# Performance work log

Measured on AMD Instinct MI355X. Metric: run time of the kernel, lower is better.

The kernel has to match this reference:

```python
import jax, jax.numpy as jnp
import numpy as np


def setup_inputs() -> dict:
    key = jax.random.key(0)
    ks = jax.random.split(key, 6)
    B, S, DK = 4, 2048, 1024
    scale = 1.0 / np.sqrt(DK)  # keep weight magnitudes sane like torch init
    return {
        "q": jax.random.normal(ks[0], (B, S, DK), jnp.float32),
        "k": jax.random.normal(ks[1], (B, S, DK), jnp.float32),
        "v": jax.random.normal(ks[2], (B, S, DK), jnp.float32),
        "wq": jax.random.normal(ks[3], (DK, DK), jnp.float32) * scale,
        "wk": jax.random.normal(ks[4], (DK, DK), jnp.float32) * scale,
        "wv": jax.random.normal(ks[5], (DK, DK), jnp.float32) * scale,
    }


def reference(q, k, v, wq, wk, wv):
    dk = q.shape[-1]
    # nn.Linear: y = x @ W^T  (weights stored [out, in])
    qp = jnp.einsum("bsd,ed->bse", q, wq)
    kp = jnp.einsum("bsd,ed->bse", k, wk)
    vp = jnp.einsum("bsd,ed->bse", v, wv)
    norm = 1.0 / jnp.sqrt(jnp.asarray(dk, qp.dtype))
    s = jnp.einsum("bqd,bkd->bqk", qp, kp) * norm  # [B, S, S]
    # module computes exp(s)/sum(exp(s)) manually; mathematically softmax
    e = jnp.exp(s)
    attention = e / jnp.sum(e, axis=-1, keepdims=True)
    # dropout is identity in eval mode (deterministic reference)
    return jnp.einsum("bqk,bkd->bqd", attention, vp)
```

## Files before the change

kernel.cpp:

```cpp
#include <hip/hip_runtime.h>

typedef _Float16 f16;
typedef _Float16 f16x4 __attribute__((ext_vector_type(4)));
typedef _Float16 f16x8 __attribute__((ext_vector_type(8)));
typedef float    fx4   __attribute__((ext_vector_type(4)));

#define MODE_PROJ   0
#define MODE_SCORES 1
#define MODE_PV     2

constexpr int Bsz = 4;
constexpr int S   = 2048;
constexpr int DK  = 1024;
constexpr int BM = 128, BN = 128, BK = 64;
constexpr long SD   = (long)S * DK;
constexpr long SS   = (long)S * S;
constexpr long BIGN = (long)Bsz * S * DK;

__device__ __forceinline__ void glds16(const f16* g, f16* l) {
    __builtin_amdgcn_global_load_lds(
        (const __attribute__((address_space(1))) void*)g,
        (__attribute__((address_space(3))) void*)l, 16, 0, 0);
}

template<int SH>
__device__ __forceinline__ size_t pp(int r, int c) {
    return ((size_t)(r >> 1) << SH) + ((r & 1) << 10) + c;
}

__global__ __launch_bounds__(256)
void convert_kernel(const float* q, const float* k, const float* v,
                    const float* wq, const float* wk, const float* wv,
                    f16* dq, f16* dk, f16* dv,
                    f16* dwq, f16* dwk, f16* dwv,
                    int sh, int inplace, float* rowsum)
{
    const int tid = threadIdx.x;
    if (blockIdx.x < 8) {
        float4 zz = {0.f, 0.f, 0.f, 0.f};
        *(float4*)&rowsum[(blockIdx.x * 256 + tid) * 4] = zz;
    }
    float4 f0[4], f1[4];
    f16* dst[4];
    size_t doff[4];
    #pragma unroll
    for (int i = 0; i < 4; ++i) {
        int cx = blockIdx.x + i * 3456;
        const float* s; f16* d; int blk;
        if (cx < 12288) {
            int t = cx >> 12; blk = cx & 4095;
            s = (t == 0) ? q : (t == 1) ? k : v;
            d = (t == 0) ? dq : (t == 1) ? dk : dv;
        } else {
            int u = cx - 12288;
            int t = u >> 9; blk = u & 511;
            s = (t == 0) ? wq : (t == 1) ? wk : wv;
            d = (t == 0) ? dwq : (t == 1) ? dwk : dwv;
        }
        size_t off = (size_t)blk * 2048 + (size_t)tid * 8;
        f0[i] = *(const float4*)(s + off);
        f1[i] = *(const float4*)(s + off + 4);
        dst[i]  = d;
        doff[i] = ((size_t)blk << (sh + 1)) + (size_t)tid * 16;
    }
    if (inplace) __syncthreads();
    #pragma unroll
    for (int i = 0; i < 4; ++i) {
        f16x8 h = {(f16)f0[i].x, (f16)f0[i].y, (f16)f0[i].z, (f16)f0[i].w,
                   (f16)f1[i].x, (f16)f1[i].y, (f16)f1[i].z, (f16)f1[i].w};
        *(f16x8*)((char*)dst[i] + doff[i]) = h;
    }
}

template<int MODE, int SH>
__global__ __launch_bounds__(256, 4)
void gemm_kernel(const f16* A0, const f16* A1, const f16* A2,
                 const f16* B0, const f16* B1, const f16* B2,
                 void* O0, void* O1, float* rowsum,
                 int lda, int ldb, int K, int ldo, int zz)
{
    __shared__ f16 lA[BM * BK];
    __shared__ f16 lB[BN * BK];

    const int tid = threadIdx.x;
    int id, z;
    if constexpr (MODE == MODE_PROJ) {
        id = blockIdx.x;
        z  = (zz >= 0) ? zz : (int)blockIdx.y;
    } else {
        constexpr int PB = (MODE == MODE_SCORES) ? 256 : 128;
        int f = blockIdx.x;
        int g = (f & 7) * ((PB * Bsz) >> 3) + (f >> 3);
        z  = g / PB;
        id = g % PB;
    }
    int row0, col0;
    if constexpr (MODE == MODE_PROJ) { row0 = (id & 63) * BM; col0 = (id >> 6) * BN; }
    else                             { row0 = (id & 15) * BM; col0 = (id >> 4) * BN; }

    const int lane = tid & 63;
    const int quad = lane >> 4;
    const int cn   = lane & 15;
    const int w    = tid >> 6;
    const int wm   = w >> 1;
    const int wn   = w & 1;

    const f16 *Ap, *Bp;
    if constexpr (MODE == MODE_PROJ) {
        Ap = (z == 0) ? A0 : (z == 1) ? A1 : A2;
        Bp = (z == 0) ? B0 : (z == 1) ? B1 : B2;
    } else if constexpr (MODE == MODE_SCORES) {
        Ap = A0 + (long)z * SD;  Bp = B0 + (long)z * SD;
        rowsum += (long)z * S;
    } else {
        Ap = A0 + (long)z * SS;  Bp = B0 + (long)z * SD;
        rowsum += (long)z * S;
    }

    fx4 acc[4][4];
    #pragma unroll
    for (int mt = 0; mt < 4; ++mt)
        #pragma unroll
        for (int nt = 0; nt < 4; ++nt)
            acc[mt][nt] = (fx4){0.f, 0.f, 0.f, 0.f};

    const int lr8 = lane >> 3;
    const int swc = (lane & 7) ^ lr8;
    const int lcS = swc << 3;

    for (int k0 = 0; k0 < K; k0 += BK) {
        __syncthreads();
        #pragma unroll
        for (int i = 0; i < 4; ++i) {
            int rb = w * 32 + i * 8;
            if constexpr (MODE == MODE_PROJ) {
                glds16(Ap + pp<SH>(row0 + rb + lr8, k0 + lcS), &lA[rb * BK]);
                glds16(Bp + pp<SH>(col0 + rb + lr8, k0 + lcS), &lB[rb * BK]);
            } else {
                glds16(Ap + (size_t)(row0 + rb + lr8) * lda + k0 + lcS, &lA[rb * BK]);
                glds16(Bp + (size_t)(col0 + rb + lr8) * ldb + k0 + lcS, &lB[rb * BK]);
            }
        }
        __syncthreads();

        #pragma unroll
        for (int kh = 0; kh < 2; ++kh) {
            f16x8 af[4], bf[4];
            #pragma unroll
            for (int mt = 0; mt < 4; ++mt) {
                int r = wm * 64 + mt * 16 + cn;
                int ch = ((kh << 2) | quad) ^ (r & 7);
                af[mt] = *(const f16x8*)&lA[r * BK + ch * 8];
            }
            #pragma unroll
            for (int nt = 0; nt < 4; ++nt) {
                int r = wn * 64 + nt * 16 + cn;
                int ch = ((kh << 2) | quad) ^ (r & 7);
                bf[nt] = *(const f16x8*)&lB[r * BK + ch * 8];
            }
            #pragma unroll
            for (int mt = 0; mt < 4; ++mt)
                #pragma unroll
                for (int nt = 0; nt < 4; ++nt)
                    acc[mt][nt] = __builtin_amdgcn_mfma_f32_16x16x32_f16(
                        af[mt], bf[nt], acc[mt][nt], 0, 0, 0);
        }
    }

    if constexpr (MODE == MODE_PROJ) {
        if (z < 2) {
            f16* O = (f16*)O0 + (long)z * BIGN;
            #pragma unroll
            for (int mt = 0; mt < 4; ++mt) {
                int r0 = row0 + wm * 64 + mt * 16 + quad * 4;
                #pragma unroll
                for (int nt = 0; nt < 4; ++nt) {
                    int c = col0 + wn * 64 + nt * 16 + cn;
                    #pragma unroll
                    for (int reg = 0; reg < 4; ++reg)
                        O[(size_t)(r0 + reg) * DK + c] = (f16)acc[mt][nt][reg];
                }
            }
        } else {
            #pragma unroll
            for (int mt = 0; mt < 4; ++mt) {
                int r0 = row0 + wm * 64 + mt * 16 + quad * 4;
                int b  = r0 >> 11;
                int s  = r0 & 2047;
                f16* O = (f16*)O1 + (long)b * SD;
                #pragma unroll
                for (int nt = 0; nt < 4; ++nt) {
                    int c = col0 + wn * 64 + nt * 16 + cn;
                    f16x4 h = {(f16)acc[mt][nt][0], (f16)acc[mt][nt][1],
                               (f16)acc[mt][nt][2], (f16)acc[mt][nt][3]};
                    *(f16x4*)&O[(size_t)c * S + s] = h;
                }
            }
        }
    } else if constexpr (MODE == MODE_SCORES) {
        f16* O = (f16*)O0 + (long)z * SS;
        const float sl2e = 0.03125f * 1.44269504f;
        float rs[4][4];
        #pragma unroll
        for (int mt = 0; mt < 4; ++mt)
            #pragma unroll
            for (int reg = 0; reg < 4; ++reg) rs[mt][reg] = 0.f;
        #pragma unroll
        for (int mt = 0; mt < 4; ++mt) {
            int r0 = row0 + wm * 64 + mt * 16 + quad * 4;
            #pragma unroll
            for (int nt = 0; nt < 4; ++nt) {
                int c = col0 + wn * 64 + nt * 16 + cn;
                #pragma unroll
                for (int reg = 0; reg < 4; ++reg) {
                    float vv = exp2f(acc[mt][nt][reg] * sl2e);
                    rs[mt][reg] += vv;
                    O[(size_t)(r0 + reg) * ldo + c] = (f16)vv;
                }
            }
        }
        #pragma unroll
        for (int mt = 0; mt < 4; ++mt) {
            int r0 = row0 + wm * 64 + mt * 16 + quad * 4;
            #pragma unroll
            for (int reg = 0; reg < 4; ++reg) {
                float vv = rs[mt][reg];
                vv += __shfl_xor(vv, 1);
                vv += __shfl_xor(vv, 2);
                vv += __shfl_xor(vv, 4);
                vv += __shfl_xor(vv, 8);
                if (cn == 0) atomicAdd(&rowsum[r0 + reg], vv);
            }
        }
    } else {
        float* O = (float*)O0 + (long)z * SD;
        #pragma unroll
        for (int mt = 0; mt < 4; ++mt) {
            int r0 = row0 + wm * 64 + mt * 16 + quad * 4;
            fx4 rsv = *(const fx4*)&rowsum[r0];
            fx4 inv = {1.f / rsv[0], 1.f / rsv[1], 1.f / rsv[2], 1.f / rsv[3]};
            #pragma unroll
            for (int nt = 0; nt < 4; ++nt) {
                int c = col0 + wn * 64 + nt * 16 + cn;
                #pragma unroll
                for (int reg = 0; reg < 4; ++reg)
                    O[(size_t)(r0 + reg) * ldo + c] = acc[mt][nt][reg] * inv[reg];
            }
        }
    }
}

extern "C" void kernel_launch(void* const* d_in, const int* in_sizes, int n_in,
                              void* d_out, int out_size, void* d_ws, size_t ws_size,
                              hipStream_t stream) {
    const float* q  = (const float*)d_in[0];
    const float* k  = (const float*)d_in[1];
    const float* v  = (const float*)d_in[2];
    const float* wq = (const float*)d_in[3];
    const float* wk = (const float*)d_in[4];
    const float* wv = (const float*)d_in[5];
    float* out = (float*)d_out;

    char* ws = (char*)d_ws;
    f16*   qp     = (f16*)(ws);
    f16*   kp     = (f16*)(ws + ((size_t)16 << 20));
    f16*   vpT    = (f16*)(ws + ((size_t)32 << 20));
    f16*   E      = (f16*)(ws + ((size_t)48 << 20));
    float* rowsum = (float*)(ws + ((size_t)80 << 20));

    const bool usews = ws_size >= ((size_t)135 << 20);
    char* cb = ws + ((size_t)81 << 20);
    f16 *dq, *dk, *dv, *dwq, *dwk, *dwv;
    if (usews) {
        dq  = (f16*)(cb);
        dk  = (f16*)(cb + ((size_t)16 << 20));
        dv  = (f16*)(cb + ((size_t)32 << 20));
        dwq = (f16*)(cb + ((size_t)48 << 20));
        dwk = (f16*)(cb + ((size_t)50 << 20));
        dwv = (f16*)(cb + ((size_t)52 << 20));
    } else {
        dq  = (f16*)q;  dk  = (f16*)k;  dv  = (f16*)v;
        dwq = (f16*)wq; dwk = (f16*)wk; dwv = (f16*)wv;
    }

    convert_kernel<<<3456, 256, 0, stream>>>(
        q, k, v, wq, wk, wv, dq, dk, dv, dwq, dwk, dwv,
        usews ? 11 : 12, usews ? 0 : 1, rowsum);

    dim3 blk(256);
    if (usews) {
        gemm_kernel<MODE_PROJ, 11><<<512, blk, 0, stream>>>(
            dq, dk, dv, dwq, dwk, dwv, qp, vpT, nullptr, DK, DK, DK, DK, 0);
        gemm_kernel<MODE_PROJ, 11><<<512, blk, 0, stream>>>(
            dq, dk, dv, dwq, dwk, dwv, qp, vpT, nullptr, DK, DK, DK, DK, 1);
        gemm_kernel<MODE_PROJ, 11><<<512, blk, 0, stream>>>(
            dq, dk, dv, dwq, dwk, dwv, qp, vpT, nullptr, DK, DK, DK, DK, 2);
    } else {
        gemm_kernel<MODE_PROJ, 12><<<512, blk, 0, stream>>>(
            dq, dk, dv, dwq, dwk, dwv, qp, vpT, nullptr, DK, DK, DK, DK, 0);
        gemm_kernel<MODE_PROJ, 12><<<512, blk, 0, stream>>>(
            dq, dk, dv, dwq, dwk, dwv, qp, vpT, nullptr, DK, DK, DK, DK, 1);
        gemm_kernel<MODE_PROJ, 12><<<512, blk, 0, stream>>>(
            dq, dk, dv, dwq, dwk, dwv, qp, vpT, nullptr, DK, DK, DK, DK, 2);
    }
    gemm_kernel<MODE_SCORES, 12><<<1024, blk, 0, stream>>>(
        qp, nullptr, nullptr, kp, nullptr, nullptr, E, nullptr, rowsum,
        DK, DK, DK, S, -1);
    gemm_kernel<MODE_PV, 12><<<512, blk, 0, stream>>>(
        E, nullptr, nullptr, vpT, nullptr, nullptr, out, nullptr, rowsum,
        S, S, S, DK, -1);
}
```

Baseline: 305.6 us.

## Fuse fp32-to-fp16 conversion of activations into projection GEMM A-tile loads

Removes the separate conversion pass over q/k/v by having the projection GEMM load fp32 activations directly into registers, convert them, and store them into LDS, with a one-tile register prefetch. Only the weights are now pre-converted by a smaller kernel, which also zeroes rowsum. This cuts the large write and reread of fp16 activation copies, in exchange for register-staged A loads and doubled fp32 read bytes per A tile, which is re-read across column blocks.

```diff
diff --git a/kernel.cpp b/kernel.cpp
--- a/kernel.cpp
+++ b/kernel.cpp
@@ -26,6 +26,36 @@
 template<int SH>
 __device__ __forceinline__ size_t pp(int r, int c) {
     return ((size_t)(r >> 1) << SH) + ((r & 1) << 10) + c;
+}
+
+__global__ __launch_bounds__(256)
+void convert_w_kernel(const float* wq, const float* wk, const float* wv,
+                      f16* dwq, f16* dwk, f16* dwv, float* rowsum)
+{
+    const int tid = threadIdx.x;
+    const int bid = blockIdx.x;
+    if (bid < 8) {
+        float4 zz = {0.f, 0.f, 0.f, 0.f};
+        *(float4*)&rowsum[(bid * 256 + tid) * 4] = zz;
+    }
+    float4 fv[4];
+    f16*   dp[4];
+    #pragma unroll
+    for (int i = 0; i < 4; ++i) {
+        unsigned g = (unsigned)(i * 196608 + bid * 256 + tid);
+        unsigned t = g >> 18;
+        unsigned off = g & 262143u;
+        const float* s = (t == 0) ? wq : (t == 1) ? wk : wv;
+        f16* d = (t == 0) ? dwq : (t == 1) ? dwk : dwv;
+        fv[i] = *(const float4*)(s + (size_t)off * 4);
+        dp[i] = d + (size_t)off * 4;
+    }
+    __builtin_amdgcn_sched_barrier(0);
+    #pragma unroll
+    for (int i = 0; i < 4; ++i) {
+        f16x4 h = {(f16)fv[i].x, (f16)fv[i].y, (f16)fv[i].z, (f16)fv[i].w};
+        *(f16x4*)dp[i] = h;
+    }
 }
 
 __global__ __launch_bounds__(256)
@@ -72,15 +102,16 @@
     }
 }
 
-template<int MODE, int SH>
+template<int MODE, int SH, int AF32>
 __global__ __launch_bounds__(256, 4)
 void gemm_kernel(const f16* A0, const f16* A1, const f16* A2,
                  const f16* B0, const f16* B1, const f16* B2,
+                 const float* F0, const float* F1, const float* F2,
                  void* O0, void* O1, float* rowsum,
                  int lda, int ldb, int K, int ldo, int zz)
 {
-    __shared__ f16 lA[BM * BK];
-    __shared__ f16 lB[BN * BK];
+    __shared__ __attribute__((aligned(16))) f16 lA[BM * BK];
+    __shared__ __attribute__((aligned(16))) f16 lB[BN * BK];
 
     const int tid = threadIdx.x;
     int id, z;
@@ -105,9 +136,11 @@
     const int wm   = w >> 1;
     const int wn   = w & 1;
 
-    const f16 *Ap, *Bp;
+    const f16 *Ap = nullptr, *Bp = nullptr;
+    const float *Fp = nullptr;
     if constexpr (MODE == MODE_PROJ) {
-        Ap = (z == 0) ? A0 : (z == 1) ? A1 : A2;
+        if constexpr (AF32) Fp = (z == 0) ? F0 : (z == 1) ? F1 : F2;
+        else                Ap = (z == 0) ? A0 : (z == 1) ? A1 : A2;
         Bp = (z == 0) ? B0 : (z == 1) ? B1 : B2;
     } else if constexpr (MODE == MODE_SCORES) {
         Ap = A0 + (long)z * SD;  Bp = B0 + (long)z * SD;
@@ -128,20 +161,52 @@
     const int swc = (lane & 7) ^ lr8;
     const int lcS = swc << 3;
 
+    float4 pfa[8];
+#define LOADA(K0) do {                                                       \
+    _Pragma("unroll")                                                        \
+    for (int i_ = 0; i_ < 4; ++i_) {                                         \
+        const float* sp_ = Fp + (size_t)(row0 + w * 32 + i_ * 8 + lr8) * DK  \
+                              + (K0) + lcS;                                  \
+        pfa[2 * i_]     = *(const float4*)sp_;                               \
+        pfa[2 * i_ + 1] = *(const float4*)(sp_ + 4);                         \
+    }                                                                        \
+} while (0)
+
+    if constexpr (MODE == MODE_PROJ && AF32) LOADA(0);
+
     for (int k0 = 0; k0 < K; k0 += BK) {
         __syncthreads();
-        #pragma unroll
-        for (int i = 0; i < 4; ++i) {
-            int rb = w * 32 + i * 8;
-            if constexpr (MODE == MODE_PROJ) {
-                glds16(Ap + pp<SH>(row0 + rb + lr8, k0 + lcS), &lA[rb * BK]);
+        if constexpr (MODE == MODE_PROJ && AF32) {
+            #pragma unroll
+            for (int i = 0; i < 4; ++i) {
+                int rb = w * 32 + i * 8;
+                float4 a = pfa[2 * i], b = pfa[2 * i + 1];
+                f16x8 h = {(f16)a.x, (f16)a.y, (f16)a.z, (f16)a.w,
+                           (f16)b.x, (f16)b.y, (f16)b.z, (f16)b.w};
+                *(f16x8*)&lA[(rb + lr8) * BK + (lane & 7) * 8] = h;
                 glds16(Bp + pp<SH>(col0 + rb + lr8, k0 + lcS), &lB[rb * BK]);
-            } else {
-                glds16(Ap + (size_t)(row0 + rb + lr8) * lda + k0 + lcS, &lA[rb * BK]);
-                glds16(Bp + (size_t)(col0 + rb + lr8) * ldb + k0 + lcS, &lB[rb * BK]);
+            }
+        } else {
+            #pragma unroll
+            for (int i = 0; i < 4; ++i) {
+                int rb = w * 32 + i * 8;
+                if constexpr (MODE == MODE_PROJ) {
+                    glds16(Ap + pp<SH>(row0 + rb + lr8, k0 + lcS), &lA[rb * BK]);
+                    glds16(Bp + pp<SH>(col0 + rb + lr8, k0 + lcS), &lB[rb * BK]);
+                } else {
+                    glds16(Ap + (size_t)(row0 + rb + lr8) * lda + k0 + lcS, &lA[rb * BK]);
+                    glds16(Bp + (size_t)(col0 + rb + lr8) * ldb + k0 + lcS, &lB[rb * BK]);
+                }
             }
         }
         __syncthreads();
+
+        if constexpr (MODE == MODE_PROJ && AF32) {
+            if (k0 + BK < K) {
+                LOADA(k0 + BK);
+                __builtin_amdgcn_sched_barrier(0);
+            }
+        }
 
         #pragma unroll
         for (int kh = 0; kh < 2; ++kh) {
@@ -166,6 +231,7 @@
                         af[mt], bf[nt], acc[mt][nt], 0, 0, 0);
         }
     }
+#undef LOADA
 
     if constexpr (MODE == MODE_PROJ) {
         if (z < 2) {
@@ -268,45 +334,44 @@
     f16*   E      = (f16*)(ws + ((size_t)48 << 20));
     float* rowsum = (float*)(ws + ((size_t)80 << 20));
 
-    const bool usews = ws_size >= ((size_t)135 << 20);
+    const bool usews = ws_size >= ((size_t)90 << 20);
     char* cb = ws + ((size_t)81 << 20);
-    f16 *dq, *dk, *dv, *dwq, *dwk, *dwv;
-    if (usews) {
-        dq  = (f16*)(cb);
-        dk  = (f16*)(cb + ((size_t)16 << 20));
-        dv  = (f16*)(cb + ((size_t)32 << 20));
-        dwq = (f16*)(cb + ((size_t)48 << 20));
-        dwk = (f16*)(cb + ((size_t)50 << 20));
-        dwv = (f16*)(cb + ((size_t)52 << 20));
-    } else {
-        dq  = (f16*)q;  dk  = (f16*)k;  dv  = (f16*)v;
-        dwq = (f16*)wq; dwk = (f16*)wk; dwv = (f16*)wv;
-    }
-
-    convert_kernel<<<3456, 256, 0, stream>>>(
-        q, k, v, wq, wk, wv, dq, dk, dv, dwq, dwk, dwv,
-        usews ? 11 : 12, usews ? 0 : 1, rowsum);
+    f16* dwq = (f16*)(cb);
+    f16* dwk = (f16*)(cb + ((size_t)2 << 20));
+    f16* dwv = (f16*)(cb + ((size_t)4 << 20));
 
     dim3 blk(256);
     if (usews) {
-        gemm_kernel<MODE_PROJ, 11><<<512, blk, 0, stream>>>(
-            dq, dk, dv, dwq, dwk, dwv, qp, vpT, nullptr, DK, DK, DK, DK, 0);
-        gemm_kernel<MODE_PROJ, 11><<<512, blk, 0, stream>>>(
-            dq, dk, dv, dwq, dwk, dwv, qp, vpT, nullptr, DK, DK, DK, DK, 1);
-        gemm_kernel<MODE_PROJ, 11><<<512, blk, 0, stream>>>(
-            dq, dk, dv, dwq, dwk, dwv, qp, vpT, nullptr, DK, DK, DK, DK, 2);
+        convert_w_kernel<<<768, blk, 0, stream>>>(
+            wq, wk, wv, dwq, dwk, dwv, rowsum);
+        gemm_kernel<MODE_PROJ, 11, 1><<<512, blk, 0, stream>>>(
+            nullptr, nullptr, nullptr, dwq, dwk, dwv, q, k, v,
+            qp, vpT, nullptr, DK, DK, DK, DK, 0);
+        gemm_kernel<MODE_PROJ, 11, 1><<<512, blk, 0, stream>>>(
+            nullptr, nullptr, nullptr, dwq, dwk, dwv, q, k, v,
+            qp, vpT, nullptr, DK, DK, DK, DK, 1);
+        gemm_kernel<MODE_PROJ, 11, 1><<<512, blk, 0, stream>>>(
+            nullptr, nullptr, nullptr, dwq, dwk, dwv, q, k, v,
+            qp, vpT, nullptr, DK, DK, DK, DK, 2);
     } else {
-        gemm_kernel<MODE_PROJ, 12><<<512, blk, 0, stream>>>(
-            dq, dk, dv, dwq, dwk, dwv, qp, vpT, nullptr, DK, DK, DK, DK, 0);
-        gemm_kernel<MODE_PROJ, 12><<<512, blk, 0, stream>>>(
-            dq, dk, dv, dwq, dwk, dwv, qp, vpT, nullptr, DK, DK, DK, DK, 1);
-        gemm_kernel<MODE_PROJ, 12><<<512, blk, 0, stream>>>(
-            dq, dk, dv, dwq, dwk, dwv, qp, vpT, nullptr, DK, DK, DK, DK, 2);
-    }
-    gemm_kernel<MODE_SCORES, 12><<<1024, blk, 0, stream>>>(
-        qp, nullptr, nullptr, kp, nullptr, nullptr, E, nullptr, rowsum,
-        DK, DK, DK, S, -1);
-    gemm_kernel<MODE_PV, 12><<<512, blk, 0, stream>>>(
-        E, nullptr, nullptr, vpT, nullptr, nullptr, out, nullptr, rowsum,
-        S, S, S, DK, -1);
-}
+        f16* dq = (f16*)q;  f16* dk = (f16*)k;  f16* dv = (f16*)v;
+        f16* iwq = (f16*)wq; f16* iwk = (f16*)wk; f16* iwv = (f16*)wv;
+        convert_kernel<<<3456, blk, 0, stream>>>(
+            q, k, v, wq, wk, wv, dq, dk, dv, iwq, iwk, iwv, 12, 1, rowsum);
+        gemm_kernel<MODE_PROJ, 12, 0><<<512, blk, 0, stream>>>(
+            dq, dk, dv, iwq, iwk, iwv, nullptr, nullptr, nullptr,
+            qp, vpT, nullptr, DK, DK, DK, DK, 0);
+        gemm_kernel<MODE_PROJ, 12, 0><<<512, blk, 0, stream>>>(
+            dq, dk, dv, iwq, iwk, iwv, nullptr, nullptr, nullptr,
+            qp, vpT, nullptr, DK, DK, DK, DK, 1);
+        gemm_kernel<MODE_PROJ, 12, 0><<<512, blk, 0, stream>>>(
+            dq, dk, dv, iwq, iwk, iwv, nullptr, nullptr, nullptr,
+            qp, vpT, nullptr, DK, DK, DK, DK, 2);
+    }
+    gemm_kernel<MODE_SCORES, 12, 0><<<1024, blk, 0, stream>>>(
+        qp, nullptr, nullptr, kp, nullptr, nullptr, nullptr, nullptr, nullptr,
+        E, nullptr, rowsum, DK, DK, DK, S, -1);
+    gemm_kernel<MODE_PV, 12, 0><<<512, blk, 0, stream>>>(
+        E, nullptr, nullptr, vpT, nullptr, nullptr, nullptr, nullptr, nullptr,
+        out, nullptr, rowsum, S, S, S, DK, -1);
+}
```

After: 367.5 us. 20.2% more time.
